# Kernel optimization log

Measured on AMD Instinct MI355X. Metric: run time of the kernel, lower is better.

## Reference

```python
import jax, jax.numpy as jnp
import numpy as np

HEAD_SIZE = 64
EMBED_DIM = 1024
N_HEAD = EMBED_DIM // HEAD_SIZE
BATCH, SEQ = 8, 2048


def wkv6(r, k, v, w, u, s):
    # r,k,v,w: (B,T,H,D); u: (H,D); s: (B,H,D,D) indexed state[j,i] (j: key dim, i: value dim)
    decay = jnp.exp(-jnp.exp(w))  # RWKV-6 CUDA kernel computes exp(-exp(w)) per channel/step

    def step(state, inp):
        r_t, k_t, v_t, d_t = inp  # each (B,H,D)
        kv = k_t[..., :, None] * v_t[..., None, :]  # (B,H,D,D)
        y_t = jnp.einsum('bhj,bhji->bhi', r_t, state + u[..., :, None] * kv)
        state = d_t[..., :, None] * state + kv
        return state, y_t

    xs = tuple(jnp.moveaxis(t, 1, 0) for t in (r, k, v, decay))  # time-major (T,B,H,D)
    s_final, y = jax.lax.scan(step, s, xs)
    return jnp.moveaxis(y, 0, 1), s_final  # (B,T,H,D), (B,H,D,D)


def setup_inputs() -> dict:
    key = jax.random.key(0)
    ks = jax.random.split(key, 20)
    C, H, D = EMBED_DIM, N_HEAD, HEAD_SIZE
    f = jnp.float32
    inp = {
        'x': jax.random.normal(ks[0], (BATCH, SEQ, C), f),
        'x_last': jax.random.normal(ks[1], (BATCH, SEQ, C), f),
        's': jnp.zeros((BATCH, H, D, D), f),
        'miu_x': jax.random.uniform(ks[2], (1, 1, C), f),
        'lambda_': jax.random.uniform(ks[3], (5, 1, 1, C), f),
        'A': jax.random.normal(ks[4], (C, 160), f) * 0.01,
        'B_lora': jax.random.normal(ks[5], (5, 32, C), f) * 0.01,
        'time_decay_miu': jax.random.uniform(ks[6], (1, 1, C), f, minval=-6.0, maxval=-0.5),
        'td_A': jax.random.normal(ks[7], (C, 64), f) * 0.01,
        'td_B': jax.random.normal(ks[8], (64, C), f) * 0.01,
        'u': jax.random.normal(ks[9], (H, D), f) * 0.5,
        'W_k': jax.random.normal(ks[10], (C, C), f) * (0.05 / C ** 0.5),
        'W_v': jax.random.normal(ks[11], (C, C), f) * (0.5 / C ** 0.5),
        'W_r': jax.random.normal(ks[12], (C, C), f) * (0.5 / C ** 0.5),
        'W_o': jax.random.normal(ks[13], (C, C), f) * (0.5 / C ** 0.5),
        'W_g1': jax.random.normal(ks[14], (C, 160), f) * 0.01,
        'W_g2': jax.random.normal(ks[15], (160, C), f) * 0.01,
        'gn_gamma': jnp.ones((C,), f),
        'gn_beta': jnp.zeros((C,), f),
    }
    return inp


def reference(x, x_last, s, miu_x, lambda_, A, B_lora, time_decay_miu, td_A, td_B, u,
              W_k, W_v, W_r, W_o, W_g1, W_g2, gn_gamma, gn_beta):
    Bsz, T, C = x.shape
    H, D = C // HEAD_SIZE, HEAD_SIZE
    x_raw = x
    # ddlerp: token-shift mix with data-dependent mus from batched LoRA
    b_a = x_last - x
    xl = x + b_a * miu_x
    # NB: source uses a raw .view(5, B*T, 32) (no transpose) -- replicate exactly with reshape
    t1 = jnp.tanh(xl @ A).reshape(5, Bsz * T, 32)
    miu = lambda_ + jnp.einsum('fmk,fkc->fmc', t1, B_lora).reshape(5, Bsz, T, C)
    xdd = x[None] + b_a[None] * miu  # (5,B,T,C)
    w0, k0, v0, r0, g0 = xdd[0], xdd[1], xdd[2], xdd[3], xdd[4]
    # decay LoRA
    w = time_decay_miu + jnp.tanh(w0 @ td_A) @ td_B  # (B,T,C)
    k = (k0 @ W_k.T) * jnp.exp(jnp.minimum(w, 0.0))
    v = v0 @ W_v.T
    r = r0 @ W_r.T
    g = jnp.tanh(g0 @ W_g1) @ W_g2
    rh, kh, vh, wh = (t.reshape(Bsz, T, H, D) for t in (r, k, v, w))
    y, s_new = wkv6(rh, kh, vh, wh, u, s)
    # GroupNorm over (B*T, n_head groups of head_size), eps = 1e-5 * n_head
    y = y.reshape(Bsz * T, H, D)
    eps = 1e-5 * H
    mu = y.mean(axis=-1, keepdims=True)
    var = y.var(axis=-1, keepdims=True)
    yn = (y - mu) / jnp.sqrt(var + eps)
    yn = yn * gn_gamma.reshape(H, D) + gn_beta.reshape(H, D)
    yn = yn.reshape(Bsz, T, C)
    out = (yn * g) @ W_o.T
    return out, x_raw, s_new
```

## Files before the change

### kernel.cpp

```cpp
#include <hip/hip_runtime.h>
#include <hip/hip_bf16.h>

namespace {

typedef __attribute__((ext_vector_type(8))) short short8x;
typedef __attribute__((ext_vector_type(4))) float f32x4;

__device__ __forceinline__ float bf2f(unsigned short h) {
    return __uint_as_float(((unsigned int)h) << 16);
}
__device__ __forceinline__ unsigned short f2bf(float f) {
    __hip_bfloat16 h = __float2bfloat16(f);
    return *reinterpret_cast<unsigned short*>(&h);
}
__device__ __forceinline__ void gload16(const unsigned short* g, unsigned short* l) {
    __builtin_amdgcn_global_load_lds(
        (const __attribute__((address_space(1))) void*)g,
        (__attribute__((address_space(3))) void*)l, 16, 0, 0);
}

enum { ACT_NONE = 0, ACT_TANH = 1 };
enum { EPI_NONE = 0, EPI_KSCALE = 1, EPI_ADDVEC = 2 };

template <int ACT, int EPI, int SBF>
__launch_bounds__(256) __global__
void gemm_mfma(int Npad, int K, int Nreal, int Cstride,
               const unsigned short* __restrict__ A,
               const unsigned short* __restrict__ B,
               float* __restrict__ Cf, unsigned short* __restrict__ Cb,
               const float* __restrict__ epi)
{
    __shared__ unsigned short as_[128 * 32];
    __shared__ unsigned short bs_[128 * 32];
    const int tid = threadIdx.x;
    const int lane = tid & 63;
    const int wave = tid >> 6;
    const int m0 = blockIdx.y << 7;
    const int n0 = blockIdx.x << 7;
    const int wm = (wave >> 1) << 6;
    const int wn = (wave & 1) << 6;

    f32x4 acc[4][4];
    const f32x4 zero = {0.f, 0.f, 0.f, 0.f};
#pragma unroll
    for (int i = 0; i < 4; ++i)
#pragma unroll
        for (int j = 0; j < 4; ++j) acc[i][j] = zero;

    const int grow = lane >> 2;
    const int gcol = (lane & 3) << 3;
    const unsigned short* a0p = A + (size_t)(m0 + (wave << 5) + grow) * K + gcol;
    const unsigned short* a1p = A + (size_t)(m0 + (wave << 5) + 16 + grow) * K + gcol;
    const unsigned short* b0p = B + (size_t)(n0 + (wave << 5) + grow) * K + gcol;
    const unsigned short* b1p = B + (size_t)(n0 + (wave << 5) + 16 + grow) * K + gcol;
    unsigned short* la0 = as_ + (wave * 2 + 0) * 512;
    unsigned short* la1 = as_ + (wave * 2 + 1) * 512;
    unsigned short* lb0 = bs_ + (wave * 2 + 0) * 512;
    unsigned short* lb1 = bs_ + (wave * 2 + 1) * 512;

    for (int k0 = 0; k0 < K; k0 += 32) {
        __syncthreads();
        gload16(a0p + k0, la0);
        gload16(b0p + k0, lb0);
        gload16(a1p + k0, la1);
        gload16(b1p + k0, lb1);
        __syncthreads();
        const int q = lane >> 4;
        const int l15 = lane & 15;
        short8x af[4], bfr[4];
#pragma unroll
        for (int i = 0; i < 4; ++i) {
            af[i]  = *(const short8x*)&as_[(wm + (i << 4) + l15) * 32 + q * 8];
            bfr[i] = *(const short8x*)&bs_[(wn + (i << 4) + l15) * 32 + q * 8];
        }
#pragma unroll
        for (int i = 0; i < 4; ++i)
#pragma unroll
            for (int j = 0; j < 4; ++j)
                acc[i][j] = __builtin_amdgcn_mfma_f32_16x16x32_bf16(af[i], bfr[j], acc[i][j], 0, 0, 0);
    }

    const int q = lane >> 4;
    const int cn = lane & 15;
#pragma unroll
    for (int i = 0; i < 4; ++i) {
#pragma unroll
        for (int j = 0; j < 4; ++j) {
#pragma unroll
            for (int rr = 0; rr < 4; ++rr) {
                const int row = m0 + wm + (i << 4) + (q << 2) + rr;
                const int col = n0 + wn + (j << 4) + cn;
                if (col >= Nreal) continue;
                float v = acc[i][j][rr];
                if constexpr (ACT == ACT_TANH) v = tanhf(v);
                if constexpr (EPI == EPI_KSCALE)
                    v *= __expf(fminf(epi[(size_t)row * 1024 + col], 0.f));
                if constexpr (EPI == EPI_ADDVEC) v += epi[col];
                if constexpr (SBF) Cb[(size_t)row * Cstride + col] = f2bf(v);
                else               Cf[(size_t)row * Cstride + col] = v;
            }
        }
    }
}

__launch_bounds__(256) __global__
void mix_k(const float* __restrict__ x, const float* __restrict__ xla,
           const float* __restrict__ mux, unsigned short* __restrict__ out)
{
    const size_t idx = ((size_t)blockIdx.x * 256 + threadIdx.x) * 4;
    const int c = (int)(idx & 1023);
    const float4 xv = *(const float4*)(x + idx);
    const float4 xl = *(const float4*)(xla + idx);
    const float4 mu = *(const float4*)(mux + c);
    ushort4 o;
    o.x = f2bf(xv.x + (xl.x - xv.x) * mu.x);
    o.y = f2bf(xv.y + (xl.y - xv.y) * mu.y);
    o.z = f2bf(xv.z + (xl.z - xv.z) * mu.z);
    o.w = f2bf(xv.w + (xl.w - xv.w) * mu.w);
    *(ushort4*)(out + idx) = o;
}

__launch_bounds__(256) __global__
void convert_k(const float* __restrict__ src, unsigned short* __restrict__ dst)
{
    const size_t idx = ((size_t)blockIdx.x * 256 + threadIdx.x) * 4;
    const float4 v = *(const float4*)(src + idx);
    ushort4 o;
    o.x = f2bf(v.x); o.y = f2bf(v.y); o.z = f2bf(v.z); o.w = f2bf(v.w);
    *(ushort4*)(dst + idx) = o;
}

__launch_bounds__(256) __global__
void transpose_k(const float* __restrict__ src, unsigned short* __restrict__ dst,
                 int K, int Nsrc)
{
    const int k = blockIdx.x * 256 + threadIdx.x;
    const int n = blockIdx.y;
    if (k < K)
        dst[(size_t)n * K + k] = (n < Nsrc) ? f2bf(src[(size_t)k * Nsrc + n]) : (unsigned short)0;
}

__launch_bounds__(256) __global__
void xdd_k(const float* __restrict__ x, const float* __restrict__ xla,
           const unsigned short* __restrict__ t1, const float* __restrict__ blora,
           const float* __restrict__ lam, unsigned short* __restrict__ out, int f)
{
    __shared__ float sh[4][32];
    const int tid = threadIdx.x;
    const int m0 = blockIdx.x << 2;
    if (tid < 128) {
        const int r = tid >> 5, kk = tid & 31;
        sh[r][kk] = bf2f(t1[(size_t)f * 524288 + (size_t)(m0 + r) * 32 + kk]);
    }
    __syncthreads();
    const int c0 = tid << 2;
    const float* bl = blora + f * 32768 + c0;
    float dot[4][4];
#pragma unroll
    for (int r = 0; r < 4; ++r)
#pragma unroll
        for (int j = 0; j < 4; ++j) dot[r][j] = 0.f;
    for (int kk = 0; kk < 32; ++kk) {
        const float4 b4 = *(const float4*)(bl + (size_t)kk * 1024);
#pragma unroll
        for (int r = 0; r < 4; ++r) {
            const float tv = sh[r][kk];
            dot[r][0] = fmaf(tv, b4.x, dot[r][0]);
            dot[r][1] = fmaf(tv, b4.y, dot[r][1]);
            dot[r][2] = fmaf(tv, b4.z, dot[r][2]);
            dot[r][3] = fmaf(tv, b4.w, dot[r][3]);
        }
    }
    const float4 l4 = *(const float4*)(lam + f * 1024 + c0);
#pragma unroll
    for (int r = 0; r < 4; ++r) {
        const size_t idx = (size_t)(m0 + r) * 1024 + c0;
        const float4 xv = *(const float4*)(x + idx);
        const float4 xl = *(const float4*)(xla + idx);
        ushort4 o;
        o.x = f2bf(xv.x + (xl.x - xv.x) * (l4.x + dot[r][0]));
        o.y = f2bf(xv.y + (xl.y - xv.y) * (l4.y + dot[r][1]));
        o.z = f2bf(xv.z + (xl.z - xv.z) * (l4.z + dot[r][2]));
        o.w = f2bf(xv.w + (xl.w - xv.w) * (l4.w + dot[r][3]));
        *(ushort4*)(out + idx) = o;
    }
}

__launch_bounds__(256) __global__
void decay_k(float* __restrict__ p)
{
    const size_t idx = ((size_t)blockIdx.x * 256 + threadIdx.x) * 4;
    const float4 v = *(const float4*)(p + idx);
    float4 o;
    o.x = __expf(-__expf(v.x));
    o.y = __expf(-__expf(v.y));
    o.z = __expf(-__expf(v.z));
    o.w = __expf(-__expf(v.w));
    *(float4*)(p + idx) = o;
}

#define BF_LO(x) __uint_as_float((x) << 16)
#define BF_HI(x) __uint_as_float((x) & 0xFFFF0000u)

#define WKV_LOAD(RV, KV, DV, VVv, T0)                                         \
    do {                                                                      \
        _Pragma("unroll")                                                     \
        for (int tt = 0; tt < 4; ++tt) {                                      \
            const size_t o_ = (size_t)((T0) + tt) * 1024;                     \
            RV[tt] = *(const uint4*)(rp + o_);                                \
            KV[tt] = *(const uint4*)(kp + o_);                                \
            DV[tt][0] = *(const float4*)(dp + o_);                            \
            DV[tt][1] = *(const float4*)(dp + o_ + 4);                        \
            VVv[tt] = vp[o_];                                                 \
        }                                                                     \
    } while (0)

#define P3_COMP(RV, KV, DV, VVv, SLOT, TH)                                    \
    do {                                                                      \
        _Pragma("unroll")                                                     \
        for (int tt = 0; tt < 4; ++tt) {                                      \
            const float vi_ = bf2f(VVv[tt]);                                  \
            float rj[8], kj[8], dj[8];                                        \
            rj[0] = BF_LO(RV[tt].x); rj[1] = BF_HI(RV[tt].x);                 \
            rj[2] = BF_LO(RV[tt].y); rj[3] = BF_HI(RV[tt].y);                 \
            rj[4] = BF_LO(RV[tt].z); rj[5] = BF_HI(RV[tt].z);                 \
            rj[6] = BF_LO(RV[tt].w); rj[7] = BF_HI(RV[tt].w);                 \
            kj[0] = BF_LO(KV[tt].x); kj[1] = BF_HI(KV[tt].x);                 \
            kj[2] = BF_LO(KV[tt].y); kj[3] = BF_HI(KV[tt].y);                 \
            kj[4] = BF_LO(KV[tt].z); kj[5] = BF_HI(KV[tt].z);                 \
            kj[6] = BF_LO(KV[tt].w); kj[7] = BF_HI(KV[tt].w);                 \
            dj[0] = DV[tt][0].x; dj[1] = DV[tt][0].y;                         \
            dj[2] = DV[tt][0].z; dj[3] = DV[tt][0].w;                         \
            dj[4] = DV[tt][1].x; dj[5] = DV[tt][1].y;                         \
            dj[6] = DV[tt][1].z; dj[7] = DV[tt][1].w;                         \
            float ya0_ = 0.f, ya1_ = 0.f;                                     \
            _Pragma("unroll")                                                 \
            for (int jj = 0; jj < 8; ++jj) {                                  \
                const float t_ = kj[jj] * vi_;                                \
                const float a_ = fmaf(u8[jj], t_, s[jj]);                     \
                if (jj & 1) ya1_ = fmaf(rj[jj], a_, ya1_);                    \
                else        ya0_ = fmaf(rj[jj], a_, ya0_);                    \
                s[jj] = fmaf(dj[jj], s[jj], t_);                              \
            }                                                                 \
            red[SLOT][w][(TH) * 4 + tt][l] = ya0_ + ya1_;                     \
        }                                                                     \
    } while (0)

#define P1_LOAD(KV, DV, VVv, T0)                                              \
    do {                                                                      \
        _Pragma("unroll")                                                     \
        for (int tt = 0; tt < 4; ++tt) {                                      \
            const size_t o_ = (size_t)((T0) + tt) * 1024;                     \
            KV[tt] = *(const uint4*)(kp + o_);                                \
            DV[tt][0] = *(const float4*)(dp + o_);                            \
            DV[tt][1] = *(const float4*)(dp + o_ + 4);                       \
            VVv[tt] = vp[o_];                                                 \
        }                                                                     \
    } while (0)

#define P1_PROC(KV, DV, VVv)                                                  \
    do {                                                                      \
        _Pragma("unroll")                                                     \
        for (int tt = 0; tt < 4; ++tt) {                                      \
            const float vi_ = bf2f(VVv[tt]);                                  \
            float kj[8], dj[8];                                               \
            kj[0] = BF_LO(KV[tt].x); kj[1] = BF_HI(KV[tt].x);                 \
            kj[2] = BF_LO(KV[tt].y); kj[3] = BF_HI(KV[tt].y);                 \
            kj[4] = BF_LO(KV[tt].z); kj[5] = BF_HI(KV[tt].z);                 \
            kj[6] = BF_LO(KV[tt].w); kj[7] = BF_HI(KV[tt].w);                 \
            dj[0] = DV[tt][0].x; dj[1] = DV[tt][0].y;                         \
            dj[2] = DV[tt][0].z; dj[3] = DV[tt][0].w;                         \
            dj[4] = DV[tt][1].x; dj[5] = DV[tt][1].y;                         \
            dj[6] = DV[tt][1].z; dj[7] = DV[tt][1].w;                         \
            _Pragma("unroll")                                                 \
            for (int jj = 0; jj < 8; ++jj) {                                  \
                const float t_ = kj[jj] * vi_;                                \
                s[jj] = fmaf(dj[jj], s[jj], t_);                              \
            }                                                                 \
        }                                                                     \
    } while (0)

__launch_bounds__(64) __global__
void wkv_p1(const unsigned short* __restrict__ k, const unsigned short* __restrict__ v,
            const float* __restrict__ d, float* __restrict__ slocal)
{
    const int blk = blockIdx.x;
    const int bh = blk & 127;
    const int jc = (blk >> 7) & 7;
    const int tc = blk >> 10;
    const int h = bh & 15;
    const int l = threadIdx.x;
    const int jbase = jc << 3;

    float s[8];
#pragma unroll
    for (int jj = 0; jj < 8; ++jj) s[jj] = 0.f;

    const size_t base = (size_t)(bh >> 4) * (2048 * 1024) + (size_t)tc * 131072 + (h << 6);
    const unsigned short* kp = k + base + jbase;
    const float*          dp = d + base + jbase;
    const unsigned short* vp = v + base + l;

    uint4 kA[4]; float4 dA[4][2]; unsigned short vA[4];
    uint4 kB[4]; float4 dB[4][2]; unsigned short vB[4];

    P1_LOAD(kA, dA, vA, 0);
    for (int c = 0; c < 32; c += 2) {
        P1_LOAD(kB, dB, vB, (c + 1) * 4);
        P1_PROC(kA, dA, vA);
        if (c + 2 < 32) P1_LOAD(kA, dA, vA, (c + 2) * 4);
        P1_PROC(kB, dB, vB);
    }
    const size_t cb = (size_t)(tc * 128 + bh) * 64 + jbase;
#pragma unroll
    for (int jj = 0; jj < 8; ++jj) slocal[(cb + jj) * 64 + l] = s[jj];
}

__launch_bounds__(64) __global__
void dprod_k(const float* __restrict__ d, float* __restrict__ dprod)
{
    const int blk = blockIdx.x;
    const int bh = blk & 127;
    const int tc = blk >> 7;
    const int h = bh & 15;
    const int l = threadIdx.x;
    const size_t base = (size_t)(bh >> 4) * (2048 * 1024) + (size_t)tc * 131072 + (h << 6) + l;
    float d0 = 1.f, d1 = 1.f, d2 = 1.f, d3 = 1.f;
    for (int t = 0; t < 128; t += 4) {
        d0 *= d[base + (size_t)t * 1024];
        d1 *= d[base + (size_t)(t + 1) * 1024];
        d2 *= d[base + (size_t)(t + 2) * 1024];
        d3 *= d[base + (size_t)(t + 3) * 1024];
    }
    dprod[(size_t)blk * 64 + l] = (d0 * d1) * (d2 * d3);
}

__launch_bounds__(64) __global__
void wkv_p2(const float* __restrict__ s_in, const float* __restrict__ slocal,
            const float* __restrict__ dprod, float* __restrict__ sstart,
            float* __restrict__ s_out)
{
    const int blk = blockIdx.x;
    const int bh = blk & 127;
    const int jc = blk >> 7;
    const int l = threadIdx.x;
    const int jbase = jc << 3;

    float s[8];
    const size_t sb = (size_t)bh * 4096;
#pragma unroll
    for (int jj = 0; jj < 8; ++jj) s[jj] = s_in[sb + (size_t)(jbase + jj) * 64 + l];

    for (int c = 0; c < 16; ++c) {
        const size_t cb = (size_t)(c * 128 + bh) * 64 + jbase;
#pragma unroll
        for (int jj = 0; jj < 8; ++jj) sstart[(cb + jj) * 64 + l] = s[jj];
#pragma unroll
        for (int jj = 0; jj < 8; ++jj)
            s[jj] = fmaf(dprod[cb + jj], s[jj], slocal[(cb + jj) * 64 + l]);
    }
#pragma unroll
    for (int jj = 0; jj < 8; ++jj) s_out[sb + (size_t)(jbase + jj) * 64 + l] = s[jj];
}

__launch_bounds__(512) __global__
void wkv_p3(const unsigned short* __restrict__ r, const unsigned short* __restrict__ k,
            const unsigned short* __restrict__ v, const float* __restrict__ d,
            const float* __restrict__ u, const float* __restrict__ sstart,
            float* __restrict__ y)
{
    const int blk = blockIdx.x;
    const int bh = blk & 127;
    const int tc = blk >> 7;
    const int h = bh & 15;
    const int tid = threadIdx.x;
    const int w = tid >> 6;
    const int l = tid & 63;
    const int jbase = w << 3;

    __shared__ float red[2][8][8][64];

    float s[8];
    const size_t cb = (size_t)(tc * 128 + bh) * 64 + jbase;
#pragma unroll
    for (int jj = 0; jj < 8; ++jj) s[jj] = sstart[(cb + jj) * 64 + l];

    float u8[8];
#pragma unroll
    for (int jj = 0; jj < 8; ++jj) u8[jj] = u[(h << 6) + jbase + jj];

    const size_t base = (size_t)(bh >> 4) * (2048 * 1024) + (size_t)tc * 131072 + (h << 6);
    const unsigned short* rp = r + base + jbase;
    const unsigned short* kp = k + base + jbase;
    const float*          dp = d + base + jbase;
    const unsigned short* vp = v + base + l;
    float*                yp = y + base + l;

    uint4 rA[4], kA[4]; float4 dA[4][2]; unsigned short vA[4];
    uint4 rB[4], kB[4]; float4 dB[4][2]; unsigned short vB[4];

    WKV_LOAD(rA, kA, dA, vA, 0);
    for (int g = 0; g < 16; ++g) {
        const int t0 = g * 8;
        WKV_LOAD(rB, kB, dB, vB, t0 + 4);
        P3_COMP(rA, kA, dA, vA, g & 1, 0);
        if (g + 1 < 16) WKV_LOAD(rA, kA, dA, vA, t0 + 8);
        P3_COMP(rB, kB, dB, vB, g & 1, 1);
        __syncthreads();
        float acc_ = red[g & 1][0][w][l];
#pragma unroll
        for (int w_ = 1; w_ < 8; ++w_) acc_ += red[g & 1][w_][w][l];
        yp[(size_t)(t0 + w) * 1024] = acc_;
    }
}

__launch_bounds__(256) __global__
void gn_k(const float* __restrict__ y0,
          const unsigned short* __restrict__ g, const float* __restrict__ gam,
          const float* __restrict__ bet, unsigned short* __restrict__ z)
{
    const int tid = threadIdx.x;
    const size_t row = blockIdx.x;
    const int c0 = tid << 2;
    const size_t idx = row * 1024 + c0;
    const float4 a = *(const float4*)(y0 + idx);
    const float yv0 = a.x, yv1 = a.y, yv2 = a.z, yv3 = a.w;
    float sm = yv0 + yv1 + yv2 + yv3;
    float q = yv0 * yv0 + yv1 * yv1 + yv2 * yv2 + yv3 * yv3;
#pragma unroll
    for (int off = 1; off < 16; off <<= 1) {
        sm += __shfl_xor(sm, off, 64);
        q += __shfl_xor(q, off, 64);
    }
    const float mean = sm * (1.f / 64.f);
    const float var = q * (1.f / 64.f) - mean * mean;
    const float rstd = rsqrtf(var + 1.6e-4f);
    const float4 gm = *(const float4*)(gam + c0);
    const float4 bt = *(const float4*)(bet + c0);
    const ushort4 gg = *(const ushort4*)(g + idx);
    ushort4 o;
    o.x = f2bf(((yv0 - mean) * rstd * gm.x + bt.x) * bf2f(gg.x));
    o.y = f2bf(((yv1 - mean) * rstd * gm.y + bt.y) * bf2f(gg.y));
    o.z = f2bf(((yv2 - mean) * rstd * gm.z + bt.z) * bf2f(gg.z));
    o.w = f2bf(((yv3 - mean) * rstd * gm.w + bt.w) * bf2f(gg.w));
    *(ushort4*)(z + idx) = o;
}

__launch_bounds__(256) __global__
void copy_k(const float4* __restrict__ src, float4* __restrict__ dst)
{
    const size_t i = (size_t)blockIdx.x * 256 + threadIdx.x;
    dst[i] = src[i];
}

}

extern "C" void kernel_launch(void* const* d_in, const int* in_sizes, int n_in,
                              void* d_out, int out_size, void* d_ws, size_t ws_size,
                              hipStream_t stream)
{
    (void)in_sizes; (void)n_in; (void)out_size; (void)ws_size;
    const float* x     = (const float*)d_in[0];
    const float* xla   = (const float*)d_in[1];
    const float* s_in  = (const float*)d_in[2];
    const float* mux   = (const float*)d_in[3];
    const float* lam   = (const float*)d_in[4];
    const float* Amat  = (const float*)d_in[5];
    const float* blora = (const float*)d_in[6];
    const float* tdmu  = (const float*)d_in[7];
    const float* tdA   = (const float*)d_in[8];
    const float* tdB   = (const float*)d_in[9];
    const float* u     = (const float*)d_in[10];
    const float* Wk    = (const float*)d_in[11];
    const float* Wv    = (const float*)d_in[12];
    const float* Wr    = (const float*)d_in[13];
    const float* Wo    = (const float*)d_in[14];
    const float* Wg1   = (const float*)d_in[15];
    const float* Wg2   = (const float*)d_in[16];
    const float* gam   = (const float*)d_in[17];
    const float* bet   = (const float*)d_in[18];

    float* out  = (float*)d_out;
    float* xraw = out + 16777216;
    float* snew = out + 2 * 16777216;

    char* ws = (char*)d_ws;
    unsigned short* mixb   = (unsigned short*)(ws);
    unsigned short* xddb   = (unsigned short*)(ws + 33554432);
    unsigned short* t1     = (unsigned short*)(ws + 67108864);
    unsigned short* tanh64 = (unsigned short*)(ws + 72351744);
    unsigned short* tanhg  = (unsigned short*)(ws + 74448896);
    unsigned short* kbuf   = (unsigned short*)(ws + 79691776);
    unsigned short* vbuf   = (unsigned short*)(ws + 113246208);
    unsigned short* rbuf   = (unsigned short*)(ws + 146800640);
    unsigned short* gbuf   = (unsigned short*)(ws + 180355072);
    unsigned short* wkt    = (unsigned short*)(ws + 213909504);
    unsigned short* wvt    = (unsigned short*)(ws + 216006656);
    unsigned short* wrt    = (unsigned short*)(ws + 218103808);
    unsigned short* wot    = (unsigned short*)(ws + 220200960);
    unsigned short* at_    = (unsigned short*)(ws + 222298112);
    unsigned short* tdat   = (unsigned short*)(ws + 222822400);
    unsigned short* tdbt   = (unsigned short*)(ws + 223084544);
    unsigned short* wg1t   = (unsigned short*)(ws + 223215616);
    unsigned short* wg2t   = (unsigned short*)(ws + 223739904);

    float* w  = out;
    float* y0 = xraw;
    float* slocal = (float*)ws;
    float* sstart = (float*)(ws + 33554432);
    float* dprod  = (float*)(ws + 67108864);

    convert_k<<<1024, 256, 0, stream>>>(Wk, wkt);
    convert_k<<<1024, 256, 0, stream>>>(Wv, wvt);
    convert_k<<<1024, 256, 0, stream>>>(Wr, wrt);
    convert_k<<<1024, 256, 0, stream>>>(Wo, wot);
    transpose_k<<<dim3(4, 256), 256, 0, stream>>>(Amat, at_, 1024, 160);
    transpose_k<<<dim3(4, 128), 256, 0, stream>>>(tdA, tdat, 1024, 64);
    transpose_k<<<dim3(1, 1024), 256, 0, stream>>>(tdB, tdbt, 64, 1024);
    transpose_k<<<dim3(4, 256), 256, 0, stream>>>(Wg1, wg1t, 1024, 160);
    transpose_k<<<dim3(1, 1024), 256, 0, stream>>>(Wg2, wg2t, 160, 1024);

    mix_k<<<16384, 256, 0, stream>>>(x, xla, mux, mixb);
    gemm_mfma<ACT_TANH, EPI_NONE, 1><<<dim3(2, 128), 256, 0, stream>>>(
        256, 1024, 160, 160, mixb, at_, nullptr, t1, nullptr);

    xdd_k<<<4096, 256, 0, stream>>>(x, xla, t1, blora, lam, xddb, 0);
    gemm_mfma<ACT_TANH, EPI_NONE, 1><<<dim3(1, 128), 256, 0, stream>>>(
        128, 1024, 64, 64, xddb, tdat, nullptr, tanh64, nullptr);
    gemm_mfma<ACT_NONE, EPI_ADDVEC, 0><<<dim3(8, 128), 256, 0, stream>>>(
        1024, 64, 1024, 1024, tanh64, tdbt, w, nullptr, tdmu);

    xdd_k<<<4096, 256, 0, stream>>>(x, xla, t1, blora, lam, xddb, 1);
    gemm_mfma<ACT_NONE, EPI_KSCALE, 1><<<dim3(8, 128), 256, 0, stream>>>(
        1024, 1024, 1024, 1024, xddb, wkt, nullptr, kbuf, w);

    decay_k<<<16384, 256, 0, stream>>>(w);

    xdd_k<<<4096, 256, 0, stream>>>(x, xla, t1, blora, lam, xddb, 2);
    gemm_mfma<ACT_NONE, EPI_NONE, 1><<<dim3(8, 128), 256, 0, stream>>>(
        1024, 1024, 1024, 1024, xddb, wvt, nullptr, vbuf, nullptr);

    xdd_k<<<4096, 256, 0, stream>>>(x, xla, t1, blora, lam, xddb, 3);
    gemm_mfma<ACT_NONE, EPI_NONE, 1><<<dim3(8, 128), 256, 0, stream>>>(
        1024, 1024, 1024, 1024, xddb, wrt, nullptr, rbuf, nullptr);

    xdd_k<<<4096, 256, 0, stream>>>(x, xla, t1, blora, lam, xddb, 4);
    gemm_mfma<ACT_TANH, EPI_NONE, 1><<<dim3(2, 128), 256, 0, stream>>>(
        256, 1024, 160, 160, xddb, wg1t, nullptr, tanhg, nullptr);
    gemm_mfma<ACT_NONE, EPI_NONE, 1><<<dim3(8, 128), 256, 0, stream>>>(
        1024, 160, 1024, 1024, tanhg, wg2t, nullptr, gbuf, nullptr);

    wkv_p1<<<16384, 64, 0, stream>>>(kbuf, vbuf, w, slocal);
    dprod_k<<<2048, 64, 0, stream>>>(w, dprod);
    wkv_p2<<<1024, 64, 0, stream>>>(s_in, slocal, dprod, sstart, snew);
    wkv_p3<<<2048, 512, 0, stream>>>(rbuf, kbuf, vbuf, w, u, sstart, y0);

    gn_k<<<16384, 256, 0, stream>>>(y0, gbuf, gam, bet, kbuf);

    gemm_mfma<ACT_NONE, EPI_NONE, 0><<<dim3(8, 128), 256, 0, stream>>>(
        1024, 1024, 1024, 1024, kbuf, wot, out, nullptr, nullptr);

    copy_k<<<16384, 256, 0, stream>>>((const float4*)x, (float4*)xraw);
}
```

Measured before the change: 1.570 ms.

## Halve WKV chunk length and factor out the u-bonus term into a dot product

The chunked WKV scan now uses 64-step chunks instead of 128, doubling the chunk count and the parallelism in phases 1 and 3 while lengthening the sequential phase 2 carry. The u*k*v bonus term is pulled out of the inner loop: it is computed as a per-token scalar (r·(u∘k)) and added as v*scalar inside the groupnorm kernel, which trims FMAs from the hot loop. Phase 2 also writes the chunk start states in place over slocal, dropping the separate sstart buffer. The risk is a longer serial phase 2 and an extra pass over r and k.

```diff
diff --git a/kernel.cpp b/kernel.cpp
--- a/kernel.cpp
+++ b/kernel.cpp
@@ -197,6 +197,35 @@
     o.z = __expf(-__expf(v.z));
     o.w = __expf(-__expf(v.w));
     *(float4*)(p + idx) = o;
+}
+
+__launch_bounds__(256) __global__
+void rku_k(const unsigned short* __restrict__ r, const unsigned short* __restrict__ k,
+           const float* __restrict__ u, float* __restrict__ rku)
+{
+    const int idx = blockIdx.x * 256 + threadIdx.x;
+    const int t = idx & 2047;
+    const int h = (idx >> 11) & 15;
+    const int b = idx >> 15;
+    const size_t base = (size_t)(b * 2048 + t) * 1024 + (h << 6);
+    const float* up = u + (h << 6);
+    float acc0 = 0.f, acc1 = 0.f;
+#pragma unroll
+    for (int j0 = 0; j0 < 64; j0 += 8) {
+        const uint4 r8 = *(const uint4*)(r + base + j0);
+        const uint4 k8 = *(const uint4*)(k + base + j0);
+        const float4 ua = *(const float4*)(up + j0);
+        const float4 ub = *(const float4*)(up + j0 + 4);
+        acc0 = fmaf(ua.x * __uint_as_float(r8.x << 16),      __uint_as_float(k8.x << 16),      acc0);
+        acc1 = fmaf(ua.y * __uint_as_float(r8.x & 0xFFFF0000u), __uint_as_float(k8.x & 0xFFFF0000u), acc1);
+        acc0 = fmaf(ua.z * __uint_as_float(r8.y << 16),      __uint_as_float(k8.y << 16),      acc0);
+        acc1 = fmaf(ua.w * __uint_as_float(r8.y & 0xFFFF0000u), __uint_as_float(k8.y & 0xFFFF0000u), acc1);
+        acc0 = fmaf(ub.x * __uint_as_float(r8.z << 16),      __uint_as_float(k8.z << 16),      acc0);
+        acc1 = fmaf(ub.y * __uint_as_float(r8.z & 0xFFFF0000u), __uint_as_float(k8.z & 0xFFFF0000u), acc1);
+        acc0 = fmaf(ub.z * __uint_as_float(r8.w << 16),      __uint_as_float(k8.w << 16),      acc0);
+        acc1 = fmaf(ub.w * __uint_as_float(r8.w & 0xFFFF0000u), __uint_as_float(k8.w & 0xFFFF0000u), acc1);
+    }
+    rku[idx] = acc0 + acc1;
 }
 
 #define BF_LO(x) __uint_as_float((x) << 16)
@@ -237,9 +266,8 @@
             _Pragma("unroll")                                                 \
             for (int jj = 0; jj < 8; ++jj) {                                  \
                 const float t_ = kj[jj] * vi_;                                \
-                const float a_ = fmaf(u8[jj], t_, s[jj]);                     \
-                if (jj & 1) ya1_ = fmaf(rj[jj], a_, ya1_);                    \
-                else        ya0_ = fmaf(rj[jj], a_, ya0_);                    \
+                if (jj & 1) ya1_ = fmaf(rj[jj], s[jj], ya1_);                 \
+                else        ya0_ = fmaf(rj[jj], s[jj], ya0_);                 \
                 s[jj] = fmaf(dj[jj], s[jj], t_);                              \
             }                                                                 \
             red[SLOT][w][(TH) * 4 + tt][l] = ya0_ + ya1_;                     \
@@ -253,7 +281,7 @@
             const size_t o_ = (size_t)((T0) + tt) * 1024;                     \
             KV[tt] = *(const uint4*)(kp + o_);                                \
             DV[tt][0] = *(const float4*)(dp + o_);                            \
-            DV[tt][1] = *(const float4*)(dp + o_ + 4);                       \
+            DV[tt][1] = *(const float4*)(dp + o_ + 4);                        \
             VVv[tt] = vp[o_];                                                 \
         }                                                                     \
     } while (0)
@@ -296,7 +324,7 @@
 #pragma unroll
     for (int jj = 0; jj < 8; ++jj) s[jj] = 0.f;
 
-    const size_t base = (size_t)(bh >> 4) * (2048 * 1024) + (size_t)tc * 131072 + (h << 6);
+    const size_t base = (size_t)(bh >> 4) * (2048 * 1024) + (size_t)tc * 65536 + (h << 6);
     const unsigned short* kp = k + base + jbase;
     const float*          dp = d + base + jbase;
     const unsigned short* vp = v + base + l;
@@ -305,10 +333,10 @@
     uint4 kB[4]; float4 dB[4][2]; unsigned short vB[4];
 
     P1_LOAD(kA, dA, vA, 0);
-    for (int c = 0; c < 32; c += 2) {
+    for (int c = 0; c < 16; c += 2) {
         P1_LOAD(kB, dB, vB, (c + 1) * 4);
         P1_PROC(kA, dA, vA);
-        if (c + 2 < 32) P1_LOAD(kA, dA, vA, (c + 2) * 4);
+        if (c + 2 < 16) P1_LOAD(kA, dA, vA, (c + 2) * 4);
         P1_PROC(kB, dB, vB);
     }
     const size_t cb = (size_t)(tc * 128 + bh) * 64 + jbase;
@@ -324,9 +352,9 @@
     const int tc = blk >> 7;
     const int h = bh & 15;
     const int l = threadIdx.x;
-    const size_t base = (size_t)(bh >> 4) * (2048 * 1024) + (size_t)tc * 131072 + (h << 6) + l;
+    const size_t base = (size_t)(bh >> 4) * (2048 * 1024) + (size_t)tc * 65536 + (h << 6) + l;
     float d0 = 1.f, d1 = 1.f, d2 = 1.f, d3 = 1.f;
-    for (int t = 0; t < 128; t += 4) {
+    for (int t = 0; t < 64; t += 4) {
         d0 *= d[base + (size_t)t * 1024];
         d1 *= d[base + (size_t)(t + 1) * 1024];
         d2 *= d[base + (size_t)(t + 2) * 1024];
@@ -336,9 +364,8 @@
 }
 
 __launch_bounds__(64) __global__
-void wkv_p2(const float* __restrict__ s_in, const float* __restrict__ slocal,
-            const float* __restrict__ dprod, float* __restrict__ sstart,
-            float* __restrict__ s_out)
+void wkv_p2(const float* __restrict__ s_in, float* __restrict__ slocal,
+            const float* __restrict__ dprod, float* __restrict__ s_out)
 {
     const int blk = blockIdx.x;
     const int bh = blk & 127;
@@ -351,13 +378,14 @@
 #pragma unroll
     for (int jj = 0; jj < 8; ++jj) s[jj] = s_in[sb + (size_t)(jbase + jj) * 64 + l];
 
-    for (int c = 0; c < 16; ++c) {
+    for (int c = 0; c < 32; ++c) {
         const size_t cb = (size_t)(c * 128 + bh) * 64 + jbase;
 #pragma unroll
-        for (int jj = 0; jj < 8; ++jj) sstart[(cb + jj) * 64 + l] = s[jj];
-#pragma unroll
-        for (int jj = 0; jj < 8; ++jj)
-            s[jj] = fmaf(dprod[cb + jj], s[jj], slocal[(cb + jj) * 64 + l]);
+        for (int jj = 0; jj < 8; ++jj) {
+            const float sloc = slocal[(cb + jj) * 64 + l];
+            slocal[(cb + jj) * 64 + l] = s[jj];
+            s[jj] = fmaf(dprod[cb + jj], s[jj], sloc);
+        }
     }
 #pragma unroll
     for (int jj = 0; jj < 8; ++jj) s_out[sb + (size_t)(jbase + jj) * 64 + l] = s[jj];
@@ -366,8 +394,7 @@
 __launch_bounds__(512) __global__
 void wkv_p3(const unsigned short* __restrict__ r, const unsigned short* __restrict__ k,
             const unsigned short* __restrict__ v, const float* __restrict__ d,
-            const float* __restrict__ u, const float* __restrict__ sstart,
-            float* __restrict__ y)
+            const float* __restrict__ sstart, float* __restrict__ y)
 {
     const int blk = blockIdx.x;
     const int bh = blk & 127;
@@ -385,11 +412,7 @@
 #pragma unroll
     for (int jj = 0; jj < 8; ++jj) s[jj] = sstart[(cb + jj) * 64 + l];
 
-    float u8[8];
-#pragma unroll
-    for (int jj = 0; jj < 8; ++jj) u8[jj] = u[(h << 6) + jbase + jj];
-
-    const size_t base = (size_t)(bh >> 4) * (2048 * 1024) + (size_t)tc * 131072 + (h << 6);
+    const size_t base = (size_t)(bh >> 4) * (2048 * 1024) + (size_t)tc * 65536 + (h << 6);
     const unsigned short* rp = r + base + jbase;
     const unsigned short* kp = k + base + jbase;
     const float*          dp = d + base + jbase;
@@ -400,11 +423,11 @@
     uint4 rB[4], kB[4]; float4 dB[4][2]; unsigned short vB[4];
 
     WKV_LOAD(rA, kA, dA, vA, 0);
-    for (int g = 0; g < 16; ++g) {
+    for (int g = 0; g < 8; ++g) {
         const int t0 = g * 8;
         WKV_LOAD(rB, kB, dB, vB, t0 + 4);
         P3_COMP(rA, kA, dA, vA, g & 1, 0);
-        if (g + 1 < 16) WKV_LOAD(rA, kA, dA, vA, t0 + 8);
+        if (g + 1 < 8) WKV_LOAD(rA, kA, dA, vA, t0 + 8);
         P3_COMP(rB, kB, dB, vB, g & 1, 1);
         __syncthreads();
         float acc_ = red[g & 1][0][w][l];
@@ -415,16 +438,25 @@
 }
 
 __launch_bounds__(256) __global__
-void gn_k(const float* __restrict__ y0,
+void gn_k(const float* __restrict__ y0, const unsigned short* __restrict__ v,
+          const float* __restrict__ rku,
           const unsigned short* __restrict__ g, const float* __restrict__ gam,
           const float* __restrict__ bet, unsigned short* __restrict__ z)
 {
     const int tid = threadIdx.x;
     const size_t row = blockIdx.x;
+    const int b = (int)(row >> 11);
+    const int t = (int)(row & 2047);
     const int c0 = tid << 2;
+    const int h = c0 >> 6;
+    const float rk = rku[((size_t)((b << 4) + h) << 11) + t];
     const size_t idx = row * 1024 + c0;
     const float4 a = *(const float4*)(y0 + idx);
-    const float yv0 = a.x, yv1 = a.y, yv2 = a.z, yv3 = a.w;
+    const ushort4 vv = *(const ushort4*)(v + idx);
+    const float yv0 = a.x + bf2f(vv.x) * rk;
+    const float yv1 = a.y + bf2f(vv.y) * rk;
+    const float yv2 = a.z + bf2f(vv.z) * rk;
+    const float yv3 = a.w + bf2f(vv.w) * rk;
     float sm = yv0 + yv1 + yv2 + yv3;
     float q = yv0 * yv0 + yv1 * yv1 + yv2 * yv2 + yv3 * yv3;
 #pragma unroll
@@ -507,8 +539,8 @@
     float* w  = out;
     float* y0 = xraw;
     float* slocal = (float*)ws;
-    float* sstart = (float*)(ws + 33554432);
     float* dprod  = (float*)(ws + 67108864);
+    float* rku    = (float*)(ws + 72351744);
 
     convert_k<<<1024, 256, 0, stream>>>(Wk, wkt);
     convert_k<<<1024, 256, 0, stream>>>(Wv, wvt);
@@ -550,12 +582,13 @@
     gemm_mfma<ACT_NONE, EPI_NONE, 1><<<dim3(8, 128), 256, 0, stream>>>(
         1024, 160, 1024, 1024, tanhg, wg2t, nullptr, gbuf, nullptr);
 
-    wkv_p1<<<16384, 64, 0, stream>>>(kbuf, vbuf, w, slocal);
-    dprod_k<<<2048, 64, 0, stream>>>(w, dprod);
-    wkv_p2<<<1024, 64, 0, stream>>>(s_in, slocal, dprod, sstart, snew);
-    wkv_p3<<<2048, 512, 0, stream>>>(rbuf, kbuf, vbuf, w, u, sstart, y0);
-
-    gn_k<<<16384, 256, 0, stream>>>(y0, gbuf, gam, bet, kbuf);
+    wkv_p1<<<32768, 64, 0, stream>>>(kbuf, vbuf, w, slocal);
+    dprod_k<<<4096, 64, 0, stream>>>(w, dprod);
+    rku_k<<<1024, 256, 0, stream>>>(rbuf, kbuf, u, rku);
+    wkv_p2<<<1024, 64, 0, stream>>>(s_in, slocal, dprod, snew);
+    wkv_p3<<<4096, 512, 0, stream>>>(rbuf, kbuf, vbuf, w, slocal, y0);
+
+    gn_k<<<16384, 256, 0, stream>>>(y0, vbuf, rku, gbuf, gam, bet, kbuf);
 
     gemm_mfma<ACT_NONE, EPI_NONE, 0><<<dim3(8, 128), 256, 0, stream>>>(
         1024, 1024, 1024, 1024, kbuf, wot, out, nullptr, nullptr);
```

Result: no change. 1.575 ms (+0.3%).
